# Optimization experiments

Measured on AMD Instinct MI355X. Metric: run time of the kernel, lower is better.

## Reference

```python
import jax, jax.numpy as jnp
import numpy as np

N, E, D, EDIM, L, H = 50000, 800000, 128, 16, 3, 8


def setup_inputs() -> dict:
    key = jax.random.key(0)
    ks = jax.random.split(key, 16)
    inner = (L + 1) * D  # concat of input + 3 GCN layer outputs
    return {
        "x": jax.random.normal(ks[0], (N, D), jnp.float32),
        "edge_index": jax.random.randint(ks[1], (2, E), 0, N),
        "edge_attr": jax.random.normal(ks[2], (E, EDIM), jnp.float32),
        "dag_edge_index": jax.random.randint(ks[3], (2, E), 0, N),
        "W_v": jax.random.normal(ks[4], (D, D), jnp.float32) * 0.05,
        "W_qk": jax.random.normal(ks[5], (D, 2 * D), jnp.float32) * 0.05,
        "gcn_W": jax.random.normal(ks[6], (L, D, D), jnp.float32) * 0.05,
        "gcn_b": jnp.zeros((L, D), jnp.float32),
        "gcn_root": jax.random.normal(ks[7], (L, D), jnp.float32) * 0.05,
        "gcn_We": jax.random.normal(ks[8], (L, EDIM, D), jnp.float32) * 0.05,
        "gcn_be": jnp.zeros((L, D), jnp.float32),
        "bn_gamma": jnp.ones((inner,), jnp.float32),
        "bn_beta": jnp.zeros((inner,), jnp.float32),
        "W_se": jax.random.normal(ks[9], (inner, D), jnp.float32) * 0.05,
        "b_se": jnp.zeros((D,), jnp.float32),
        "W_out": jax.random.normal(ks[10], (D, D), jnp.float32) * 0.05,
        "b_out": jnp.zeros((D,), jnp.float32),
    }


def reference(x, edge_index, edge_attr, dag_edge_index, W_v, W_qk, gcn_W, gcn_b,
              gcn_root, gcn_We, gcn_be, bn_gamma, bn_beta, W_se, b_se, W_out, b_out):
    n = x.shape[0]
    row, col = edge_index[0], edge_index[1]  # source j, target i

    def gcn_layer(h, Wl, bl, root, We, be):
        h = h @ Wl + bl                                   # [N, D]
        e = edge_attr @ We + be                           # [E, D]
        deg = jax.ops.segment_sum(jnp.ones(row.shape[0], h.dtype), row, num_segments=n) + 1.0
        dis = deg ** -0.5
        norm = dis[row] * dis[col]                        # [E]
        msg = norm[:, None] * jax.nn.relu(h[row] + e)     # gather + per-edge transform
        agg = jax.ops.segment_sum(msg, col, num_segments=n)  # scatter-add at target
        return agg + jax.nn.relu(h + root) / deg[:, None]

    # StructureExtractor: 3 GCN layers, concat skip features
    xs = [x]
    h = x
    for i in range(gcn_W.shape[0]):
        h = jax.nn.relu(gcn_layer(h, gcn_W[i], gcn_b[i], gcn_root[i], gcn_We[i], gcn_be[i]))
        xs.append(h)
    xc = jnp.concatenate(xs, axis=-1)                     # [N, 4D]
    mu = xc.mean(0)
    var = xc.var(0)
    xc = (xc - mu) / jnp.sqrt(var + 1e-5) * bn_gamma + bn_beta  # BatchNorm1d (batch stats)
    x_struct = xc @ W_se + b_se                           # [N, D]

    # sparse multi-head attention over dag_rr_edge_index
    v = x @ W_v
    qk = x_struct @ W_qk
    d = x.shape[1]
    qk_src_tbl, qk_dst_tbl = qk[:, :d], qk[:, d:]         # chunk(2): (qk_j, qk_i)
    hd = d // H
    scale = hd ** -0.5
    src, dst = dag_edge_index[0], dag_edge_index[1]
    qj = qk_src_tbl[src].reshape(-1, H, hd)
    qi = qk_dst_tbl[dst].reshape(-1, H, hd)
    logits = (qi * qj).sum(-1) * scale                    # [E, H]
    m = jax.ops.segment_max(logits, dst, num_segments=n)
    p = jnp.exp(logits - m[dst])
    s = jax.ops.segment_sum(p, dst, num_segments=n)
    attn = p / s[dst]                                     # per-destination softmax
    vj = v[src].reshape(-1, H, hd)
    out = jax.ops.segment_sum(vj * attn[..., None], dst, num_segments=n).reshape(-1, d)
    return out @ W_out + b_out
```

## Files before the change

kernel.cpp:

```cpp
#include <hip/hip_runtime.h>

#define D 128
#define EDIMC 16
#define GCAP 64

typedef __attribute__((ext_vector_type(8))) short short8v;
typedef __attribute__((ext_vector_type(4))) float f32x4;
typedef __attribute__((ext_vector_type(2))) float f32x2;
typedef __attribute__((ext_vector_type(2))) _Float16 h16x2;

__device__ __forceinline__ float asf(unsigned u){ union{unsigned u; float f;} v; v.u = u; return v.f; }
__device__ __forceinline__ unsigned asu(float f){ union{float f; unsigned u;} v; v.f = f; return v.u; }
__device__ __forceinline__ unsigned short f2bf(float f){
    unsigned u = asu(f);
    unsigned r = (u + 0x7fffu + ((u >> 16) & 1u)) >> 16;
    return (unsigned short)r;
}
__device__ __forceinline__ unsigned packbf(float lo, float hi){
    return (unsigned)f2bf(lo) | ((unsigned)f2bf(hi) << 16);
}
__device__ __forceinline__ unsigned packh(float a, float b){
    union{ h16x2 h; unsigned u; } v;
    v.h = (h16x2){(_Float16)a, (_Float16)b};
    return v.u;
}
__device__ __forceinline__ h16x2 ash2(unsigned u){ union{unsigned u; h16x2 h;} v; v.u = u; return v.h; }

__global__ __launch_bounds__(256) void prep_all(
    const int* __restrict__ row, const int* __restrict__ col,
    const int* __restrict__ asrc_in, const int* __restrict__ adst,
    int E, int N, int gE, int gX, int L,
    const float* __restrict__ eattr, const float* __restrict__ x,
    const float* __restrict__ gW, const float* __restrict__ Wv,
    const float* __restrict__ Wqk, const float* __restrict__ Wout,
    const float* __restrict__ gWe, const float* __restrict__ bse,
    const float* __restrict__ Wse,
    int* __restrict__ cr, int* __restrict__ curg, int* __restrict__ curd,
    int2* __restrict__ gslot, int* __restrict__ asrcS, unsigned* __restrict__ eattrh,
    unsigned* __restrict__ xbf, unsigned* __restrict__ xc,
    unsigned short* __restrict__ gWt, unsigned short* __restrict__ Wvt,
    unsigned short* __restrict__ Woutt, unsigned* __restrict__ wpk,
    float* __restrict__ WseWqk, float* __restrict__ bconst)
{
    int b = blockIdx.x, tid = threadIdx.x;
    if(b < gE){
        int e = b*256 + tid;
        if(e >= E) return;
        const float4* s4 = (const float4*)(eattr + (size_t)e*EDIMC);
        float4 a = s4[0], bb = s4[1], cc2 = s4[2], d = s4[3];
        unsigned* dst8 = eattrh + (size_t)e*8;
        dst8[0] = packh(a.x, a.y);    dst8[1] = packh(a.z, a.w);
        dst8[2] = packh(bb.x, bb.y);  dst8[3] = packh(bb.z, bb.w);
        dst8[4] = packh(cc2.x, cc2.y);dst8[5] = packh(cc2.z, cc2.w);
        dst8[6] = packh(d.x, d.y);    dst8[7] = packh(d.z, d.w);
        int r = row[e], c = col[e];
        atomicAdd(&cr[r], 1);
        int pg = atomicAdd(&curg[c], 1);
        if(pg < GCAP) gslot[c*GCAP + pg] = make_int2(r, e);
        int s2 = asrc_in[e], d2 = adst[e];
        int pd = atomicAdd(&curd[d2], 1);
        if(pd < GCAP) asrcS[d2*GCAP + pd] = s2;
    } else if(b < gE + gX){
        int idx = (b - gE)*256 + tid;
        if(idx >= N*64) return;
        int i = idx >> 6, c2 = idx & 63;
        float a = x[(size_t)i*128 + c2*2], bb = x[(size_t)i*128 + c2*2 + 1];
        unsigned p = packbf(a, bb);
        xbf[idx] = p;
        xc[(size_t)i*256 + c2] = p;
    } else {
        int wb = b - gE - gX;
        int j = tid;
        if(wb < 384){
            int l = wb >> 7, k = wb & 127;
            if(j < 128) gWt[(size_t)l*16384 + (size_t)j*128 + k] = f2bf(gW[(size_t)l*16384 + (size_t)k*128 + j]);
        } else if(wb < 512){
            int k = wb - 384;
            if(j < 128) Wvt[(size_t)j*128 + k] = f2bf(Wv[(size_t)k*128 + j]);
        } else if(wb < 640){
            int k = wb - 512;
            if(j < 128) Woutt[(size_t)j*128 + k] = f2bf(Wout[(size_t)k*128 + j]);
        } else if(wb < 664){
            int t = wb - 640; int l = t >> 3, kk = t & 7;
            if(j < 128){
                const float* W = gWe + (size_t)l*EDIMC*D;
                wpk[(size_t)l*1024 + kk*128 + j] = packh(W[(size_t)(2*kk)*D + j], W[(size_t)(2*kk+1)*D + j]);
            }
        } else if(wb < 1176){
            int k = wb - 664;
            float acc = 0.f;
            #pragma unroll 4
            for(int c = 0; c < 128; c++)
                acc += Wse[(size_t)k*128 + c] * Wqk[(size_t)c*256 + j];
            WseWqk[(size_t)k*256 + j] = acc;
        } else {
            float acc = 0.f;
            #pragma unroll 4
            for(int c = 0; c < 128; c++)
                acc += bse[c] * Wqk[(size_t)c*256 + j];
            bconst[j] = acc;
        }
    }
}

__global__ void deg_fin2(const int* __restrict__ cr, float* __restrict__ deg,
                         float* __restrict__ dis, int N){
    int i = blockIdx.x*blockDim.x + threadIdx.x;
    if(i < N){ float d = (float)cr[i] + 1.0f; deg[i] = d; dis[i] = rsqrtf(d); }
}

template<int OUT>
__global__ __launch_bounds__(256) void gemm_mfma(
    const unsigned short* __restrict__ A, const unsigned short* __restrict__ Bt,
    const float* __restrict__ bias, void* __restrict__ Cout,
    int M, int K, int Nc)
{
    int tid = threadIdx.x;
    int wid = tid >> 6, lane = tid & 63;
    int bm = blockIdx.y*64 + wid*16;
    int bn = blockIdx.x*64;
    int lr = lane & 15;
    int kg = lane >> 4;
    int arow = bm + lr; if(arow >= M) arow = M - 1;
    f32x4 acc[4];
    #pragma unroll
    for(int i = 0; i < 4; i++) acc[i] = (f32x4){0.f,0.f,0.f,0.f};
    for(int k0 = 0; k0 < K; k0 += 32){
        short8v a = *(const short8v*)(A + (size_t)arow*K + k0 + kg*8);
        #pragma unroll
        for(int nf = 0; nf < 4; nf++){
            short8v b = *(const short8v*)(Bt + (size_t)(bn + nf*16 + lr)*K + k0 + kg*8);
            acc[nf] = __builtin_amdgcn_mfma_f32_16x16x32_bf16(a, b, acc[nf], 0, 0, 0);
        }
    }
    int crow = bm + kg*4;
    #pragma unroll
    for(int nf = 0; nf < 4; nf++){
        int col = bn + nf*16 + lr;
        float bs = bias ? bias[col] : 0.f;
        #pragma unroll
        for(int r = 0; r < 4; r++){
            int rw = crow + r;
            if(rw < M){
                float val = acc[nf][r] + bs;
                if(OUT == 1)
                    ((unsigned short*)Cout)[(size_t)rw*Nc + col] = f2bf(val);
                else if(OUT == 2)
                    ((_Float16*)Cout)[(size_t)rw*Nc + col] = (_Float16)val;
                else
                    ((float*)Cout)[(size_t)rw*Nc + col] = val;
            }
        }
    }
}

__device__ __forceinline__ void edge_acc5(
    uint4 ea0, uint4 ea1, unsigned hu, float nm,
    const unsigned* __restrict__ w0, const unsigned* __restrict__ w1,
    float be0, float be1, float& a0, float& a1)
{
    float ev0 = be0, ev1 = be1;
    unsigned ea[8] = {ea0.x, ea0.y, ea0.z, ea0.w, ea1.x, ea1.y, ea1.z, ea1.w};
    #pragma unroll
    for(int kk = 0; kk < 8; kk++){
        ev0 = __builtin_amdgcn_fdot2(ash2(ea[kk]), ash2(w0[kk]), ev0, false);
        ev1 = __builtin_amdgcn_fdot2(ash2(ea[kk]), ash2(w1[kk]), ev1, false);
    }
    float sx = fmaxf(asf(hu << 16) + ev0, 0.f);
    float sy = fmaxf(asf(hu & 0xffff0000u) + ev1, 0.f);
    a0 += nm*sx; a1 += nm*sy;
}

__global__ __launch_bounds__(256) void gcn_gather_v8(
    const unsigned* __restrict__ hlin, const int* __restrict__ curg,
    const int2* __restrict__ gslot, const unsigned* __restrict__ eattrh,
    const float* __restrict__ dis, const unsigned* __restrict__ wpk_l,
    const float* __restrict__ be, const float* __restrict__ root,
    const float* __restrict__ deg,
    unsigned* __restrict__ xc, unsigned* __restrict__ hcur, int blk, int N)
{
    __shared__ float part[2][64][2];
    int tid = threadIdx.x;
    int lane = tid & 63;
    int wv = __builtin_amdgcn_readfirstlane(tid >> 6);
    int pairIdx = wv >> 1, h = wv & 1;
    int node = blockIdx.x*2 + pairIdx;
    bool valid = node < N;
    unsigned w0[8], w1[8];
    const uint2* wp2 = (const uint2*)wpk_l;
    #pragma unroll
    for(int kk = 0; kk < 8; kk++){
        uint2 t = wp2[(size_t)kk*64 + lane];
        w0[kk] = t.x; w1[kk] = t.y;
    }
    f32x2 be2 = ((const f32x2*)be)[lane];
    float a0 = 0.f, a1 = 0.f;
    int s0 = 0, s1 = 0;
    float disn = 0.f;
    if(valid){
        disn = dis[node];
        int cnt = min(curg[node], GCAP);
        int half0 = (cnt + 1) >> 1;
        int base = node*GCAP;
        s0 = base + (h ? half0 : 0);
        s1 = base + (h ? cnt : half0);
    }
    int s = s0;
    for(; s + 4 <= s1; s += 4){
        int2 sl0 = gslot[s+0], sl1 = gslot[s+1], sl2 = gslot[s+2], sl3 = gslot[s+3];
        float d0 = dis[sl0.x], d1 = dis[sl1.x], d2 = dis[sl2.x], d3 = dis[sl3.x];
        unsigned h0 = hlin[(size_t)sl0.x*64 + lane];
        unsigned h1 = hlin[(size_t)sl1.x*64 + lane];
        unsigned h2 = hlin[(size_t)sl2.x*64 + lane];
        unsigned h3 = hlin[(size_t)sl3.x*64 + lane];
        uint4 e00 = *(const uint4*)(eattrh + (size_t)sl0.y*8);
        uint4 e01 = *(const uint4*)(eattrh + (size_t)sl0.y*8 + 4);
        uint4 e10 = *(const uint4*)(eattrh + (size_t)sl1.y*8);
        uint4 e11 = *(const uint4*)(eattrh + (size_t)sl1.y*8 + 4);
        uint4 e20 = *(const uint4*)(eattrh + (size_t)sl2.y*8);
        uint4 e21 = *(const uint4*)(eattrh + (size_t)sl2.y*8 + 4);
        uint4 e30 = *(const uint4*)(eattrh + (size_t)sl3.y*8);
        uint4 e31 = *(const uint4*)(eattrh + (size_t)sl3.y*8 + 4);
        edge_acc5(e00, e01, h0, d0*disn, w0, w1, be2.x, be2.y, a0, a1);
        edge_acc5(e10, e11, h1, d1*disn, w0, w1, be2.x, be2.y, a0, a1);
        edge_acc5(e20, e21, h2, d2*disn, w0, w1, be2.x, be2.y, a0, a1);
        edge_acc5(e30, e31, h3, d3*disn, w0, w1, be2.x, be2.y, a0, a1);
    }
    for(; s < s1; s++){
        int2 sl0 = gslot[s];
        float d0 = dis[sl0.x];
        unsigned h0 = hlin[(size_t)sl0.x*64 + lane];
        uint4 e00 = *(const uint4*)(eattrh + (size_t)sl0.y*8);
        uint4 e01 = *(const uint4*)(eattrh + (size_t)sl0.y*8 + 4);
        edge_acc5(e00, e01, h0, d0*disn, w0, w1, be2.x, be2.y, a0, a1);
    }
    if(h){ part[pairIdx][lane][0] = a0; part[pairIdx][lane][1] = a1; }
    __syncthreads();
    if(!h && valid){
        a0 += part[pairIdx][lane][0];
        a1 += part[pairIdx][lane][1];
        f32x2 rt2 = ((const f32x2*)root)[lane];
        unsigned hlu = hlin[(size_t)node*64 + lane];
        float hlx = asf(hlu << 16), hly = asf(hlu & 0xffff0000u);
        float dinv = 1.f/deg[node];
        float v0 = fmaxf(a0 + fmaxf(hlx + rt2.x, 0.f)*dinv, 0.f);
        float v1 = fmaxf(a1 + fmaxf(hly + rt2.y, 0.f)*dinv, 0.f);
        unsigned p = packbf(v0, v1);
        hcur[(size_t)node*64 + lane] = p;
        xc[(size_t)node*256 + (size_t)blk*64 + lane] = p;
    }
}

__global__ __launch_bounds__(256) void bn_stats_bf(
    const unsigned* __restrict__ xc, int N, float* __restrict__ stats)
{
    int c0 = threadIdx.x;
    int rows_per = (N + gridDim.x - 1)/gridDim.x;
    int r0 = blockIdx.x*rows_per, r1 = min(N, r0 + rows_per);
    float s0=0, q0=0, s1=0, q1=0;
    for(int r = r0; r < r1; r++){
        unsigned u = xc[(size_t)r*256 + c0];
        float a = asf(u << 16), b = asf(u & 0xffff0000u);
        s0 += a; q0 += a*a; s1 += b; q1 += b*b;
    }
    atomicAdd(&stats[2*c0+0], s0);  atomicAdd(&stats[512 + 2*c0+0], q0);
    atomicAdd(&stats[2*c0+1], s1);  atomicAdd(&stats[512 + 2*c0+1], q1);
}

__global__ void fold_all(const float* __restrict__ gamma, const float* __restrict__ beta,
                         const float* __restrict__ stats, float Ninv,
                         const float* __restrict__ WseWqk, const float* __restrict__ bconst,
                         unsigned short* __restrict__ Wqkft, float* __restrict__ bqkf)
{
    int b = blockIdx.x, t = threadIdx.x;
    if(b < 256){
        int j = b;
        #pragma unroll
        for(int half = 0; half < 2; half++){
            int k = t + half*256;
            float mu  = stats[k]*Ninv;
            float var = stats[512+k]*Ninv - mu*mu;
            float sc  = gamma[k]*rsqrtf(var + 1e-5f);
            Wqkft[(size_t)j*512 + k] = f2bf(sc * WseWqk[(size_t)k*256 + j]);
        }
    } else {
        int j = t;
        float acc = bconst[j];
        for(int k = 0; k < 512; k++){
            float mu  = stats[k]*Ninv;
            float var = stats[512+k]*Ninv - mu*mu;
            float sc  = gamma[k]*rsqrtf(var + 1e-5f);
            float sh  = beta[k] - mu*sc;
            acc += sh*WseWqk[(size_t)k*256 + j];
        }
        bqkf[j] = acc;
    }
}

__global__ __launch_bounds__(256) void attn_fused_v8(
    const unsigned* __restrict__ qk,
    const unsigned* __restrict__ v,
    const int* __restrict__ curd, const int* __restrict__ asrcS,
    unsigned* __restrict__ out, int N)
{
    int lane = threadIdx.x & 63;
    int node = __builtin_amdgcn_readfirstlane((int)((blockIdx.x*blockDim.x + threadIdx.x) >> 6));
    if(node >= N) return;
    int cnt = min(curd[node], GCAP);
    int s0 = node*GCAP, s1 = s0 + cnt;
    float o0 = 0.f, o1 = 0.f;
    if(cnt > 0){
        h16x2 qi2 = ash2(qk[(size_t)node*128 + 64 + lane]);
        float m = -INFINITY, ssum = 0.f, a0 = 0.f, a1 = 0.f;
        int s = s0;
        for(; s + 4 <= s1; s += 4){
            int sr0 = asrcS[s+0], sr1 = asrcS[s+1], sr2 = asrcS[s+2], sr3 = asrcS[s+3];
            unsigned qj[4], vv[4];
            qj[0] = qk[(size_t)sr0*128 + lane];  vv[0] = v[(size_t)sr0*64 + lane];
            qj[1] = qk[(size_t)sr1*128 + lane];  vv[1] = v[(size_t)sr1*64 + lane];
            qj[2] = qk[(size_t)sr2*128 + lane];  vv[2] = v[(size_t)sr2*64 + lane];
            qj[3] = qk[(size_t)sr3*128 + lane];  vv[3] = v[(size_t)sr3*64 + lane];
            float l[4];
            #pragma unroll
            for(int j = 0; j < 4; j++){
                float p = __builtin_amdgcn_fdot2(qi2, ash2(qj[j]), 0.f, false);
                p += __shfl_xor(p, 1);
                p += __shfl_xor(p, 2);
                p += __shfl_xor(p, 4);
                l[j] = p*0.25f;
            }
            float mc = fmaxf(fmaxf(fmaxf(l[0], l[1]), fmaxf(l[2], l[3])), m);
            float sc = __expf(m - mc);
            float p0 = __expf(l[0] - mc), p1 = __expf(l[1] - mc);
            float p2 = __expf(l[2] - mc), p3 = __expf(l[3] - mc);
            h16x2 v0 = ash2(vv[0]), v1 = ash2(vv[1]), v2 = ash2(vv[2]), v3 = ash2(vv[3]);
            ssum = ssum*sc + (p0 + p1 + p2 + p3);
            a0 = a0*sc + p0*(float)v0.x + p1*(float)v1.x + p2*(float)v2.x + p3*(float)v3.x;
            a1 = a1*sc + p0*(float)v0.y + p1*(float)v1.y + p2*(float)v2.y + p3*(float)v3.y;
            m = mc;
        }
        for(; s < s1; s++){
            int srx = asrcS[s];
            h16x2 qj2 = ash2(qk[(size_t)srx*128 + lane]);
            h16x2 v2  = ash2(v [(size_t)srx*64  + lane]);
            float p = __builtin_amdgcn_fdot2(qi2, qj2, 0.f, false);
            p += __shfl_xor(p, 1);
            p += __shfl_xor(p, 2);
            p += __shfl_xor(p, 4);
            float l = p*0.25f;
            float mn = fmaxf(m, l);
            float sc = __expf(m - mn);
            float pe = __expf(l - mn);
            ssum = ssum*sc + pe;
            a0 = a0*sc + pe*(float)v2.x;
            a1 = a1*sc + pe*(float)v2.y;
            m = mn;
        }
        float inv = 1.f/ssum;
        o0 = a0*inv; o1 = a1*inv;
    }
    out[(size_t)node*64 + lane] = packbf(o0, o1);
}

extern "C" void kernel_launch(void* const* d_in, const int* in_sizes, int n_in,
                              void* d_out, int out_size, void* d_ws, size_t ws_size,
                              hipStream_t stream)
{
    const float* x     = (const float*)d_in[0];
    const int*   ei    = (const int*)  d_in[1];
    const float* eattr = (const float*)d_in[2];
    const int*   dei   = (const int*)  d_in[3];
    const float* Wv    = (const float*)d_in[4];
    const float* Wqk   = (const float*)d_in[5];
    const float* gW    = (const float*)d_in[6];
    const float* gb    = (const float*)d_in[7];
    const float* groot = (const float*)d_in[8];
    const float* gWe   = (const float*)d_in[9];
    const float* gbe   = (const float*)d_in[10];
    const float* gamma = (const float*)d_in[11];
    const float* beta  = (const float*)d_in[12];
    const float* Wse   = (const float*)d_in[13];
    const float* bse   = (const float*)d_in[14];
    const float* Wout  = (const float*)d_in[15];
    const float* bout  = (const float*)d_in[16];

    const int N = in_sizes[0]/D;
    const int E = in_sizes[1]/2;
    const int L = in_sizes[7]/D;

    float* ws = (float*)d_ws;
    size_t o = 0;
    auto alloc = [&](size_t n){ size_t r = o; o += (n + 63) & ~(size_t)63; return r; };
    size_t f_deg   = alloc((size_t)N);
    size_t f_dis   = alloc((size_t)N);
    size_t f_hlin  = alloc((size_t)N*64);
    size_t f_hcur  = alloc((size_t)N*64);
    size_t f_xbf   = alloc((size_t)N*64);
    size_t f_xc    = alloc((size_t)N*256);
    size_t f_st    = alloc(1024);
    size_t f_cnt   = alloc((size_t)N*3);
    size_t f_gslot = alloc((size_t)N*GCAP*2);
    size_t f_asrc  = alloc((size_t)N*GCAP);
    size_t f_eah   = alloc((size_t)E*8);
    size_t f_wgt   = alloc(40960 + 64);
    size_t f_wpk   = alloc(3*1024);
    size_t f_wsq   = alloc(512*256);
    size_t f_bcn   = alloc(256);
    size_t f_wqf   = alloc(65536);
    size_t f_bqf   = alloc(256);
    size_t f_qk    = alloc((size_t)N*128);
    size_t f_vb    = alloc((size_t)N*64);
    size_t f_aout  = alloc((size_t)N*64);
    (void)ws_size;

    float* deg  = ws + f_deg;   float* dis  = ws + f_dis;
    unsigned* hlin = (unsigned*)(ws + f_hlin);
    unsigned* hcur = (unsigned*)(ws + f_hcur);
    unsigned* xbf  = (unsigned*)(ws + f_xbf);
    unsigned* xc   = (unsigned*)(ws + f_xc);
    float* stats = ws + f_st;
    int* cnts = (int*)(ws + f_cnt);
    int* cr = cnts, *curg = cnts + N, *curd = cnts + 2*N;
    int2* gslot = (int2*)(ws + f_gslot);
    int* asrcS = (int*)(ws + f_asrc);
    unsigned* eattrh = (unsigned*)(ws + f_eah);
    unsigned short* wbase = (unsigned short*)(ws + f_wgt);
    unsigned short* gWt   = wbase;
    unsigned short* Wvt   = gWt + 3*128*128;
    unsigned short* Woutt = Wvt + 128*128;
    unsigned* wpk = (unsigned*)(ws + f_wpk);
    float* WseWqk = ws + f_wsq;
    float* bconst = ws + f_bcn;
    unsigned short* Wqkft = (unsigned short*)(ws + f_wqf);
    float* bqkf = ws + f_bqf;
    unsigned* qk   = (unsigned*)(ws + f_qk);
    unsigned* vbuf = (unsigned*)(ws + f_vb);
    unsigned* aout = (unsigned*)(ws + f_aout);

    const int* e_row = ei;        const int* e_col = ei + E;
    const int* a_src = dei;       const int* a_dst = dei + E;

    dim3 blk256(256);
    int gE = (E+255)/256, gN = (N+255)/256;
    int gNode = ((size_t)N*64 + 255)/256;
    int gX = gNode;
    int gMy = (N+63)/64;
    int gPair = (N+1)/2;

    hipMemsetAsync(cnts, 0, (size_t)N*3*sizeof(int), stream);
    prep_all<<<gE + gX + 1177, blk256, 0, stream>>>(
        e_row, e_col, a_src, a_dst, E, N, gE, gX, L,
        eattr, x, gW, Wv, Wqk, Wout, gWe, bse, Wse,
        cr, curg, curd, gslot, asrcS, eattrh,
        xbf, xc, gWt, Wvt, Woutt, wpk, WseWqk, bconst);
    deg_fin2<<<gN, blk256, 0, stream>>>(cr, deg, dis, N);

    const unsigned* hin = xbf;
    for(int l = 0; l < L; l++){
        dim3 g(2, gMy);
        gemm_mfma<1><<<g, blk256, 0, stream>>>((const unsigned short*)hin, gWt + (size_t)l*D*D,
                                               gb + (size_t)l*D, hlin, N, 128, 128);
        gcn_gather_v8<<<gPair, blk256, 0, stream>>>(hlin, curg, gslot, eattrh, dis,
                                                    wpk + (size_t)l*1024, gbe + (size_t)l*D,
                                                    groot + (size_t)l*D, deg, xc, hcur, l+1, N);
        hin = hcur;
    }

    hipMemsetAsync(stats, 0, 1024*sizeof(float), stream);
    bn_stats_bf<<<1024, blk256, 0, stream>>>(xc, N, stats);
    float Ninv = 1.0f/(float)N;
    fold_all<<<257, blk256, 0, stream>>>(gamma, beta, stats, Ninv, WseWqk, bconst, Wqkft, bqkf);

    {   dim3 g(2, gMy);
        gemm_mfma<2><<<g, blk256, 0, stream>>>((const unsigned short*)xbf, Wvt, nullptr, vbuf, N, 128, 128);
    }
    {   dim3 g(4, gMy);
        gemm_mfma<2><<<g, blk256, 0, stream>>>((const unsigned short*)xc, Wqkft, bqkf, qk, N, 512, 256);
    }

    attn_fused_v8<<<gNode, blk256, 0, stream>>>(qk, vbuf, curd, asrcS, aout, N);

    {   dim3 g(2, gMy);
        gemm_mfma<0><<<g, blk256, 0, stream>>>((const unsigned short*)aout, Woutt, bout, (float*)d_out, N, 128, 128);
    }
}
```

Before: 749.0 us.

## Use LDS-tiled 128x128 MFMA GEMM and revert GCN gather to one wave per node

Replaces the register-only MFMA GEMM with a 128x128 block tile that stages A and B through shared memory in K-chunks of 64. Each wave then computes a 64x64 sub-tile, so A/B data is reused across more MFMAs and redundant global reads of B drop. Separately, the GCN gather goes back to one wave per node instead of splitting each node's edges across two waves joined by an LDS reduction. That removes the sync and partial-sum traffic but halves per-node parallelism for high-degree nodes. The larger GEMM tiles also mean fewer blocks and higher register and LDS use per block.

```diff
diff --git a/kernel.cpp b/kernel.cpp
--- a/kernel.cpp
+++ b/kernel.cpp
@@ -110,45 +110,71 @@
 }
 
 template<int OUT>
-__global__ __launch_bounds__(256) void gemm_mfma(
+__global__ __launch_bounds__(256) void gemm_lds(
     const unsigned short* __restrict__ A, const unsigned short* __restrict__ Bt,
     const float* __restrict__ bias, void* __restrict__ Cout,
     int M, int K, int Nc)
 {
+    __shared__ unsigned short As[128*64];
+    __shared__ unsigned short Bs[128*64];
     int tid = threadIdx.x;
-    int wid = tid >> 6, lane = tid & 63;
-    int bm = blockIdx.y*64 + wid*16;
-    int bn = blockIdx.x*64;
-    int lr = lane & 15;
-    int kg = lane >> 4;
-    int arow = bm + lr; if(arow >= M) arow = M - 1;
-    f32x4 acc[4];
+    int lane = tid & 63;
+    int wid = tid >> 6;
+    int bm = blockIdx.y*128, bn = blockIdx.x*128;
+    int wr = (wid >> 1)*64, wc = (wid & 1)*64;
+    int lr = lane & 15, kg = lane >> 4;
+    f32x4 acc[4][4];
     #pragma unroll
-    for(int i = 0; i < 4; i++) acc[i] = (f32x4){0.f,0.f,0.f,0.f};
-    for(int k0 = 0; k0 < K; k0 += 32){
-        short8v a = *(const short8v*)(A + (size_t)arow*K + k0 + kg*8);
+    for(int i = 0; i < 4; i++)
         #pragma unroll
-        for(int nf = 0; nf < 4; nf++){
-            short8v b = *(const short8v*)(Bt + (size_t)(bn + nf*16 + lr)*K + k0 + kg*8);
-            acc[nf] = __builtin_amdgcn_mfma_f32_16x16x32_bf16(a, b, acc[nf], 0, 0, 0);
-        }
-    }
-    int crow = bm + kg*4;
+        for(int j = 0; j < 4; j++) acc[i][j] = (f32x4){0.f,0.f,0.f,0.f};
+
+    for(int k0 = 0; k0 < K; k0 += 64){
+        #pragma unroll
+        for(int i = 0; i < 4; i++){
+            int q = tid + 256*i;
+            int row = q >> 3, c8 = (q & 7)*8;
+            int ar = bm + row; if(ar >= M) ar = M - 1;
+            *(short8v*)&As[row*64 + c8] = *(const short8v*)&A[(size_t)ar*K + k0 + c8];
+            *(short8v*)&Bs[row*64 + c8] = *(const short8v*)&Bt[(size_t)(bn + row)*K + k0 + c8];
+        }
+        __syncthreads();
+        #pragma unroll
+        for(int kk = 0; kk < 2; kk++){
+            short8v a[4], b[4];
+            #pragma unroll
+            for(int i = 0; i < 4; i++)
+                a[i] = *(const short8v*)&As[(wr + i*16 + lr)*64 + kk*32 + kg*8];
+            #pragma unroll
+            for(int j = 0; j < 4; j++)
+                b[j] = *(const short8v*)&Bs[(wc + j*16 + lr)*64 + kk*32 + kg*8];
+            #pragma unroll
+            for(int i = 0; i < 4; i++)
+                #pragma unroll
+                for(int j = 0; j < 4; j++)
+                    acc[i][j] = __builtin_amdgcn_mfma_f32_16x16x32_bf16(a[i], b[j], acc[i][j], 0, 0, 0);
+        }
+        __syncthreads();
+    }
     #pragma unroll
-    for(int nf = 0; nf < 4; nf++){
-        int col = bn + nf*16 + lr;
+    for(int j = 0; j < 4; j++){
+        int col = bn + wc + j*16 + lr;
         float bs = bias ? bias[col] : 0.f;
         #pragma unroll
-        for(int r = 0; r < 4; r++){
-            int rw = crow + r;
-            if(rw < M){
-                float val = acc[nf][r] + bs;
-                if(OUT == 1)
-                    ((unsigned short*)Cout)[(size_t)rw*Nc + col] = f2bf(val);
-                else if(OUT == 2)
-                    ((_Float16*)Cout)[(size_t)rw*Nc + col] = (_Float16)val;
-                else
-                    ((float*)Cout)[(size_t)rw*Nc + col] = val;
+        for(int i = 0; i < 4; i++){
+            int rbase = bm + wr + i*16 + kg*4;
+            #pragma unroll
+            for(int r = 0; r < 4; r++){
+                int rw = rbase + r;
+                if(rw < M){
+                    float val = acc[i][j][r] + bs;
+                    if(OUT == 1)
+                        ((unsigned short*)Cout)[(size_t)rw*Nc + col] = f2bf(val);
+                    else if(OUT == 2)
+                        ((_Float16*)Cout)[(size_t)rw*Nc + col] = (_Float16)val;
+                    else
+                        ((float*)Cout)[(size_t)rw*Nc + col] = val;
+                }
             }
         }
     }
@@ -171,7 +197,7 @@
     a0 += nm*sx; a1 += nm*sy;
 }
 
-__global__ __launch_bounds__(256) void gcn_gather_v8(
+__global__ __launch_bounds__(256) void gcn_gather_v7(
     const unsigned* __restrict__ hlin, const int* __restrict__ curg,
     const int2* __restrict__ gslot, const unsigned* __restrict__ eattrh,
     const float* __restrict__ dis, const unsigned* __restrict__ wpk_l,
@@ -179,13 +205,9 @@
     const float* __restrict__ deg,
     unsigned* __restrict__ xc, unsigned* __restrict__ hcur, int blk, int N)
 {
-    __shared__ float part[2][64][2];
-    int tid = threadIdx.x;
-    int lane = tid & 63;
-    int wv = __builtin_amdgcn_readfirstlane(tid >> 6);
-    int pairIdx = wv >> 1, h = wv & 1;
-    int node = blockIdx.x*2 + pairIdx;
-    bool valid = node < N;
+    int lane = threadIdx.x & 63;
+    int node = __builtin_amdgcn_readfirstlane((int)((blockIdx.x*blockDim.x + threadIdx.x) >> 6));
+    if(node >= N) return;
     unsigned w0[8], w1[8];
     const uint2* wp2 = (const uint2*)wpk_l;
     #pragma unroll
@@ -194,17 +216,11 @@
         w0[kk] = t.x; w1[kk] = t.y;
     }
     f32x2 be2 = ((const f32x2*)be)[lane];
+    f32x2 rt2 = ((const f32x2*)root)[lane];
+    float disn = dis[node];
+    int s0 = node*GCAP;
+    int s1 = s0 + min(curg[node], GCAP);
     float a0 = 0.f, a1 = 0.f;
-    int s0 = 0, s1 = 0;
-    float disn = 0.f;
-    if(valid){
-        disn = dis[node];
-        int cnt = min(curg[node], GCAP);
-        int half0 = (cnt + 1) >> 1;
-        int base = node*GCAP;
-        s0 = base + (h ? half0 : 0);
-        s1 = base + (h ? cnt : half0);
-    }
     int s = s0;
     for(; s + 4 <= s1; s += 4){
         int2 sl0 = gslot[s+0], sl1 = gslot[s+1], sl2 = gslot[s+2], sl3 = gslot[s+3];
@@ -234,21 +250,14 @@
         uint4 e01 = *(const uint4*)(eattrh + (size_t)sl0.y*8 + 4);
         edge_acc5(e00, e01, h0, d0*disn, w0, w1, be2.x, be2.y, a0, a1);
     }
-    if(h){ part[pairIdx][lane][0] = a0; part[pairIdx][lane][1] = a1; }
-    __syncthreads();
-    if(!h && valid){
-        a0 += part[pairIdx][lane][0];
-        a1 += part[pairIdx][lane][1];
-        f32x2 rt2 = ((const f32x2*)root)[lane];
-        unsigned hlu = hlin[(size_t)node*64 + lane];
-        float hlx = asf(hlu << 16), hly = asf(hlu & 0xffff0000u);
-        float dinv = 1.f/deg[node];
-        float v0 = fmaxf(a0 + fmaxf(hlx + rt2.x, 0.f)*dinv, 0.f);
-        float v1 = fmaxf(a1 + fmaxf(hly + rt2.y, 0.f)*dinv, 0.f);
-        unsigned p = packbf(v0, v1);
-        hcur[(size_t)node*64 + lane] = p;
-        xc[(size_t)node*256 + (size_t)blk*64 + lane] = p;
-    }
+    unsigned hlu = hlin[(size_t)node*64 + lane];
+    float hlx = asf(hlu << 16), hly = asf(hlu & 0xffff0000u);
+    float dinv = 1.f/deg[node];
+    float v0 = fmaxf(a0 + fmaxf(hlx + rt2.x, 0.f)*dinv, 0.f);
+    float v1 = fmaxf(a1 + fmaxf(hly + rt2.y, 0.f)*dinv, 0.f);
+    unsigned p = packbf(v0, v1);
+    hcur[(size_t)node*64 + lane] = p;
+    xc[(size_t)node*256 + (size_t)blk*64 + lane] = p;
 }
 
 __global__ __launch_bounds__(256) void bn_stats_bf(
@@ -298,8 +307,7 @@
 }
 
 __global__ __launch_bounds__(256) void attn_fused_v8(
-    const unsigned* __restrict__ qk,
-    const unsigned* __restrict__ v,
+    const unsigned* __restrict__ qk, const unsigned* __restrict__ v,
     const int* __restrict__ curd, const int* __restrict__ asrcS,
     unsigned* __restrict__ out, int N)
 {
@@ -444,8 +452,7 @@
     int gE = (E+255)/256, gN = (N+255)/256;
     int gNode = ((size_t)N*64 + 255)/256;
     int gX = gNode;
-    int gMy = (N+63)/64;
-    int gPair = (N+1)/2;
+    int gM128 = (N+127)/128;
 
     hipMemsetAsync(cnts, 0, (size_t)N*3*sizeof(int), stream);
     prep_all<<<gE + gX + 1177, blk256, 0, stream>>>(
@@ -457,10 +464,10 @@
 
     const unsigned* hin = xbf;
     for(int l = 0; l < L; l++){
-        dim3 g(2, gMy);
-        gemm_mfma<1><<<g, blk256, 0, stream>>>((const unsigned short*)hin, gWt + (size_t)l*D*D,
-                                               gb + (size_t)l*D, hlin, N, 128, 128);
-        gcn_gather_v8<<<gPair, blk256, 0, stream>>>(hlin, curg, gslot, eattrh, dis,
+        dim3 g(1, gM128);
+        gemm_lds<1><<<g, blk256, 0, stream>>>((const unsigned short*)hin, gWt + (size_t)l*D*D,
+                                              gb + (size_t)l*D, hlin, N, 128, 128);
+        gcn_gather_v7<<<gNode, blk256, 0, stream>>>(hlin, curg, gslot, eattrh, dis,
                                                     wpk + (size_t)l*1024, gbe + (size_t)l*D,
                                                     groot + (size_t)l*D, deg, xc, hcur, l+1, N);
         hin = hcur;
@@ -471,16 +478,16 @@
     float Ninv = 1.0f/(float)N;
     fold_all<<<257, blk256, 0, stream>>>(gamma, beta, stats, Ninv, WseWqk, bconst, Wqkft, bqkf);
 
-    {   dim3 g(2, gMy);
-        gemm_mfma<2><<<g, blk256, 0, stream>>>((const unsigned short*)xbf, Wvt, nullptr, vbuf, N, 128, 128);
-    }
-    {   dim3 g(4, gMy);
-        gemm_mfma<2><<<g, blk256, 0, stream>>>((const unsigned short*)xc, Wqkft, bqkf, qk, N, 512, 256);
+    {   dim3 g(1, gM128);
+        gemm_lds<2><<<g, blk256, 0, stream>>>((const unsigned short*)xbf, Wvt, nullptr, vbuf, N, 128, 128);
+    }
+    {   dim3 g(2, gM128);
+        gemm_lds<2><<<g, blk256, 0, stream>>>((const unsigned short*)xc, Wqkft, bqkf, qk, N, 512, 256);
     }
 
     attn_fused_v8<<<gNode, blk256, 0, stream>>>(qk, vbuf, curd, asrcS, aout, N);
 
-    {   dim3 g(2, gMy);
-        gemm_mfma<0><<<g, blk256, 0, stream>>>((const unsigned short*)aout, Woutt, bout, (float*)d_out, N, 128, 128);
-    }
-}
+    {   dim3 g(1, gM128);
+        gemm_lds<0><<<g, blk256, 0, stream>>>((const unsigned short*)aout, Woutt, bout, (float*)d_out, N, 128, 128);
+    }
+}
```

After: 620.5 us. 17.2% less time.
